# Optimization experiments

Measured on AMD Instinct MI355X. Metric: run time of the kernel, lower is better.

The kernel has to match this reference:

```python
import math
import jax, jax.numpy as jnp
import numpy as np

B, S, E, H, DK, L, NB, V, FF, C = 4, 2048, 512, 8, 64, 2, 4, 32000, 2048, 4


def _pos_encoding(seq_len, embed_dim):
    pos = np.arange(seq_len, dtype=np.float32)[:, None]
    div = np.exp(np.arange(0, embed_dim, 2, dtype=np.float32) * (-math.log(10000.0) / embed_dim))
    pe = np.zeros((seq_len, embed_dim), dtype=np.float32)
    pe[:, 0::2] = np.sin(pos * div)
    pe[:, 1::2] = np.cos(pos * div)
    return jnp.asarray(pe)


def _layernorm(x, g, b, eps=1e-5):
    m = jnp.mean(x, axis=-1, keepdims=True)
    v = jnp.mean((x - m) ** 2, axis=-1, keepdims=True)
    return (x - m) * jax.lax.rsqrt(v + eps) * g + b


def setup_inputs() -> dict:
    key = jax.random.key(0)
    ks = jax.random.split(key, 32)
    sd = 0.02
    inp = {
        "tokens": jax.random.randint(ks[0], (B, S), 0, V, dtype=jnp.int32),
        "emb": jax.random.normal(ks[1], (V, E), jnp.float32) * sd,
        # per-block stacked params (leading dim NB)
        "Wq": jax.random.normal(ks[2], (NB, E, E), jnp.float32) * sd,
        "Wk": jax.random.normal(ks[3], (NB, E, E), jnp.float32) * sd,
        "Wv": jax.random.normal(ks[4], (NB, E, E), jnp.float32) * sd,
        "Wo": jax.random.normal(ks[5], (NB, E, E), jnp.float32) * sd,
        # quantum per-head linear stacks: [NB, L, H, DK, DK] weights, [NB, L, H, DK] biases
        "qh_w": jax.random.normal(ks[6], (NB, L, H, DK, DK), jnp.float32) * 0.1,
        "qh_b": jax.random.normal(ks[7], (NB, L, H, DK), jnp.float32) * 0.01,
        "kh_w": jax.random.normal(ks[8], (NB, L, H, DK, DK), jnp.float32) * 0.1,
        "kh_b": jax.random.normal(ks[9], (NB, L, H, DK), jnp.float32) * 0.01,
        "vh_w": jax.random.normal(ks[10], (NB, L, H, DK, DK), jnp.float32) * 0.1,
        "vh_b": jax.random.normal(ks[11], (NB, L, H, DK), jnp.float32) * 0.01,
        "ln1_g": jnp.ones((NB, E), jnp.float32),
        "ln1_b": jnp.zeros((NB, E), jnp.float32),
        "ln2_g": jnp.ones((NB, E), jnp.float32),
        "ln2_b": jnp.zeros((NB, E), jnp.float32),
        "f_w1": jax.random.normal(ks[12], (NB, E, FF), jnp.float32) * sd,
        "f_b1": jnp.zeros((NB, FF), jnp.float32),
        "f_w2": jax.random.normal(ks[13], (NB, FF, E), jnp.float32) * sd,
        "f_b2": jnp.zeros((NB, E), jnp.float32),
        "cls_w": jax.random.normal(ks[14], (E, C), jnp.float32) * sd,
        "cls_b": jnp.zeros((C,), jnp.float32),
    }
    return inp


def _quantum_apply(h, w_stack, b_stack):
    # h: [B,H,S,DK]; w_stack: [L,H,DK,DK]; b_stack: [L,H,DK]
    for l in range(L):
        h = jnp.einsum("bhsd,hde->bhse", h, w_stack[l]) + b_stack[l][None, :, None, :]
    return h


def _block(x, Wq, Wk, Wv, Wo, qh_w, qh_b, kh_w, kh_b, vh_w, vh_b,
           ln1_g, ln1_b, ln2_g, ln2_b, f_w1, f_b1, f_w2, f_b2):
    b, s, _ = x.shape
    q = (x @ Wq).reshape(b, s, H, DK).transpose(0, 2, 1, 3)  # [B,H,S,DK]
    k = (x @ Wk).reshape(b, s, H, DK).transpose(0, 2, 1, 3)
    v = (x @ Wv).reshape(b, s, H, DK).transpose(0, 2, 1, 3)
    q = _quantum_apply(q, qh_w, qh_b)
    k = _quantum_apply(k, kh_w, kh_b)
    v = _quantum_apply(v, vh_w, vh_b)
    scores = jnp.einsum("bhqd,bhkd->bhqk", q, k) / math.sqrt(DK)
    attn = jax.nn.softmax(scores, axis=-1)
    out = jnp.einsum("bhqk,bhkd->bhqd", attn, v)
    out = out.transpose(0, 2, 1, 3).reshape(b, s, E) @ Wo
    x = _layernorm(x + out, ln1_g, ln1_b)
    ffn = jax.nn.relu(x @ f_w1 + f_b1) @ f_w2 + f_b2
    return _layernorm(x + ffn, ln2_g, ln2_b)


def reference(tokens, emb, Wq, Wk, Wv, Wo, qh_w, qh_b, kh_w, kh_b, vh_w, vh_b,
              ln1_g, ln1_b, ln2_g, ln2_b, f_w1, f_b1, f_w2, f_b2, cls_w, cls_b):
    x = emb[tokens]  # [B,S,E]
    x = x + _pos_encoding(S, E)[None]
    for i in range(NB):
        x = _block(x, Wq[i], Wk[i], Wv[i], Wo[i],
                   qh_w[i], qh_b[i], kh_w[i], kh_b[i], vh_w[i], vh_b[i],
                   ln1_g[i], ln1_b[i], ln2_g[i], ln2_b[i],
                   f_w1[i], f_b1[i], f_w2[i], f_b2[i])
    x = x.mean(axis=1)  # [B,E]
    return x @ cls_w + cls_b  # [B,C]
```

## Files before the change

### kernel.cpp

```cpp
#include <hip/hip_runtime.h>
#include <hip/hip_bf16.h>
#include <math.h>

#define BB 4
#define SS 2048
#define EE 512
#define HH 8
#define DKK 64
#define LL 2
#define NBB 4
#define FFF 2048
#define CC 4
#define NBSE ((size_t)BB * SS * EE)

typedef __attribute__((ext_vector_type(8))) short bf16x8;
typedef __attribute__((ext_vector_type(4))) float f32x4;
using bf16 = __hip_bfloat16;

__device__ __forceinline__ float fast_exp2(float x) { return __builtin_amdgcn_exp2f(x); }

__device__ __forceinline__ void gload16(const bf16* g, bf16* l) {
    __builtin_amdgcn_global_load_lds((const __attribute__((address_space(1))) void*)g,
                                     (__attribute__((address_space(3))) void*)l, 16, 0, 0);
}
__device__ __forceinline__ unsigned short bf16bits(float f) {
    bf16 h = __float2bfloat16(f);
    return *(unsigned short*)&h;
}

__global__ __launch_bounds__(256) void embed_kernel(const int* __restrict__ tokens,
                                                    const float* __restrict__ emb,
                                                    float* __restrict__ x,
                                                    bf16* __restrict__ xb) {
    int i = blockIdx.x * blockDim.x + threadIdx.x;
    int total = BB * SS * EE / 2;
    if (i >= total) return;
    int pi  = i & (EE / 2 - 1);
    int row = i >> 8;
    int s   = row & (SS - 1);
    int tok = tokens[row];
    int e0  = pi * 2;
    const float kln = 9.210340371976184f / (float)EE;
    float arg = (float)s * expf(-(float)e0 * kln);
    float2 ev = *(const float2*)(emb + (size_t)tok * EE + e0);
    float2 o;
    o.x = ev.x + sinf(arg);
    o.y = ev.y + cosf(arg);
    *(float2*)(x + (size_t)row * EE + e0) = o;
    xb[(size_t)row * EE + e0]     = __float2bfloat16(o.x);
    xb[(size_t)row * EE + e0 + 1] = __float2bfloat16(o.y);
}

__global__ __launch_bounds__(256) void transpose_to_bf16(const float* __restrict__ in,
                                                         bf16* __restrict__ out,
                                                         int K, int N,
                                                         size_t zstride, int row_off) {
    const float* src = in + (size_t)blockIdx.z * K * N;
    bf16* dst = out + (size_t)blockIdx.z * zstride;
    int r0 = blockIdx.y * 64, c0 = blockIdx.x * 64;
    __shared__ float tl[64][65];
    int t = threadIdx.x;
    int lr = t >> 4, lc = (t & 15) * 4;
#pragma unroll
    for (int i = 0; i < 4; i++) {
        float4 v = *(const float4*)(src + (size_t)(r0 + lr + i * 16) * N + c0 + lc);
        tl[lr + i * 16][lc + 0] = v.x;
        tl[lr + i * 16][lc + 1] = v.y;
        tl[lr + i * 16][lc + 2] = v.z;
        tl[lr + i * 16][lc + 3] = v.w;
    }
    __syncthreads();
#pragma unroll
    for (int i = 0; i < 4; i++) {
        int n = lr + i * 16;
#pragma unroll
        for (int j = 0; j < 4; j++)
            dst[(size_t)(row_off + c0 + n) * K + r0 + lc + j] = __float2bfloat16(tl[lc + j][n]);
    }
}

#define GF_RELU 1
#define GF_SCATTER3 2
#define GF_OUTBF16 4
__global__ __launch_bounds__(256) void gemm_bf16(const bf16* __restrict__ A,
                                                 const bf16* __restrict__ BT,
                                                 const float* __restrict__ bias,
                                                 void* __restrict__ C,
                                                 int M, int N, int K, int flags) {
    __shared__ __align__(16) bf16 Asm[128 * 32];
    __shared__ __align__(16) bf16 Bsm[128 * 32];
    int t = threadIdx.x;
    int l = t & 63, w = t >> 6;
    int nbx = gridDim.x;
    int lin = blockIdx.y * nbx + blockIdx.x;
    int cpx = (nbx * gridDim.y) >> 3;
    int swz = (lin & 7) * cpx + (lin >> 3);
    int bm = (swz / nbx) * 128, bn = (swz % nbx) * 128;
    int wr = (w >> 1) * 64, wc = (w & 1) * 64;
    int lr = l & 15, lg = l >> 4;
    int ca = w * 2;
    int sr = l >> 2, sk = (l & 3) * 8;
    const bf16* ga  = A  + (size_t)(bm + ca * 16 + sr) * K + sk;
    const bf16* ga2 = ga + (size_t)16 * K;
    const bf16* gb  = BT + (size_t)(bn + ca * 16 + sr) * K + sk;
    const bf16* gb2 = gb + (size_t)16 * K;

    f32x4 acc[4][4];
#pragma unroll
    for (int m = 0; m < 4; m++)
#pragma unroll
        for (int n = 0; n < 4; n++) acc[m][n] = (f32x4){0.f, 0.f, 0.f, 0.f};

    for (int k0 = 0; k0 < K; k0 += 32) {
        __syncthreads();
        gload16(ga + k0,  &Asm[ca * 512]);
        gload16(ga2 + k0, &Asm[ca * 512 + 512]);
        gload16(gb + k0,  &Bsm[ca * 512]);
        gload16(gb2 + k0, &Bsm[ca * 512 + 512]);
        __syncthreads();
        bf16x8 af[4], bfr[4];
#pragma unroll
        for (int m = 0; m < 4; m++)
            af[m] = *(const bf16x8*)&Asm[(wr + m * 16 + lr) * 32 + lg * 8];
#pragma unroll
        for (int n = 0; n < 4; n++)
            bfr[n] = *(const bf16x8*)&Bsm[(wc + n * 16 + lr) * 32 + lg * 8];
#pragma unroll
        for (int m = 0; m < 4; m++)
#pragma unroll
            for (int n = 0; n < 4; n++)
                acc[m][n] = __builtin_amdgcn_mfma_f32_16x16x32_bf16(af[m], bfr[n], acc[m][n], 0, 0, 0);
    }

#pragma unroll
    for (int m = 0; m < 4; m++) {
        int row = bm + wr + m * 16 + lg * 4;
#pragma unroll
        for (int n = 0; n < 4; n++) {
            int col = bn + wc + n * 16 + lr;
            float bv = bias ? bias[col] : 0.f;
#pragma unroll
            for (int r = 0; r < 4; r++) {
                float v = acc[m][n][r] + bv;
                if (flags & GF_RELU) v = fmaxf(v, 0.f);
                int rr = row + r;
                if (flags & GF_SCATTER3) {
                    int tsel = col >> 9;
                    int b = rr >> 11, s = rr & (SS - 1);
                    int h = (col >> 6) & 7, dk = col & 63;
                    ((bf16*)C)[tsel * NBSE + (((size_t)(b * HH + h) * SS + s) << 6) + dk] = __float2bfloat16(v);
                } else if (flags & GF_OUTBF16) {
                    ((bf16*)C)[(size_t)rr * N + col] = __float2bfloat16(v);
                } else {
                    ((float*)C)[(size_t)rr * N + col] = v;
                }
            }
        }
    }
}

__global__ __launch_bounds__(256) void gemm_bf16_m64(const bf16* __restrict__ A,
                                                     const bf16* __restrict__ BT,
                                                     const float* __restrict__ bias,
                                                     void* __restrict__ C,
                                                     int M, int N, int K, int flags) {
    __shared__ __align__(16) bf16 Asm[64 * 32];
    __shared__ __align__(16) bf16 Bsm[128 * 32];
    int t = threadIdx.x;
    int l = t & 63, w = t >> 6;
    int nbx = gridDim.x;
    int lin = blockIdx.y * nbx + blockIdx.x;
    int cpx = (nbx * gridDim.y) >> 3;
    int swz = (lin & 7) * cpx + (lin >> 3);
    int bm = (swz / nbx) * 64, bn = (swz % nbx) * 128;
    int wr = (w >> 1) * 32, wc = (w & 1) * 64;
    int lr = l & 15, lg = l >> 4;
    int ca = w * 2;
    int sr = l >> 2, sk = (l & 3) * 8;
    const bf16* ga  = A  + (size_t)(bm + w * 16 + sr) * K + sk;
    const bf16* gb  = BT + (size_t)(bn + ca * 16 + sr) * K + sk;
    const bf16* gb2 = gb + (size_t)16 * K;

    f32x4 acc[2][4];
#pragma unroll
    for (int m = 0; m < 2; m++)
#pragma unroll
        for (int n = 0; n < 4; n++) acc[m][n] = (f32x4){0.f, 0.f, 0.f, 0.f};

    for (int k0 = 0; k0 < K; k0 += 32) {
        __syncthreads();
        gload16(ga + k0,  &Asm[w * 512]);
        gload16(gb + k0,  &Bsm[ca * 512]);
        gload16(gb2 + k0, &Bsm[ca * 512 + 512]);
        __syncthreads();
        bf16x8 af[2], bfr[4];
#pragma unroll
        for (int m = 0; m < 2; m++)
            af[m] = *(const bf16x8*)&Asm[(wr + m * 16 + lr) * 32 + lg * 8];
#pragma unroll
        for (int n = 0; n < 4; n++)
            bfr[n] = *(const bf16x8*)&Bsm[(wc + n * 16 + lr) * 32 + lg * 8];
#pragma unroll
        for (int m = 0; m < 2; m++)
#pragma unroll
            for (int n = 0; n < 4; n++)
                acc[m][n] = __builtin_amdgcn_mfma_f32_16x16x32_bf16(af[m], bfr[n], acc[m][n], 0, 0, 0);
    }

#pragma unroll
    for (int m = 0; m < 2; m++) {
        int row = bm + wr + m * 16 + lg * 4;
#pragma unroll
        for (int n = 0; n < 4; n++) {
            int col = bn + wc + n * 16 + lr;
            float bv = bias ? bias[col] : 0.f;
#pragma unroll
            for (int r = 0; r < 4; r++) {
                float v = acc[m][n][r] + bv;
                if (flags & GF_RELU) v = fmaxf(v, 0.f);
                int rr = row + r;
                if (flags & GF_OUTBF16) {
                    ((bf16*)C)[(size_t)rr * N + col] = __float2bfloat16(v);
                } else {
                    ((float*)C)[(size_t)rr * N + col] = v;
                }
            }
        }
    }
}

__global__ __launch_bounds__(256) void quantum_mfma(bf16* __restrict__ qb, bf16* __restrict__ kb, bf16* __restrict__ vb,
                                                    bf16* __restrict__ vT,
                                                    const bf16* __restrict__ qwT, const bf16* __restrict__ kwT, const bf16* __restrict__ vwT,
                                                    const float* __restrict__ qbi, const float* __restrict__ kbi, const float* __restrict__ vbi) {
    __shared__ __align__(16) bf16 Hs[128 * 72];
    __shared__ __align__(16) bf16 W0s[64 * 72];
    __shared__ __align__(16) bf16 W1s[64 * 72];
    int z = blockIdx.z;
    bf16* hb       = z == 0 ? qb  : (z == 1 ? kb  : vb);
    const bf16* wT = z == 0 ? qwT : (z == 1 ? kwT : vwT);
    const float* bi = z == 0 ? qbi : (z == 1 ? kbi : vbi);
    int bh = blockIdx.y, h = bh & (HH - 1);
    int s0 = blockIdx.x * 128;
    int t = threadIdx.x, l = t & 63, w = t >> 6;
    int lr = l & 15, lg = l >> 4;
    bf16* base = hb + ((size_t)bh * SS + s0) * DKK;
    const bf16* w0p = wT + (size_t)h * 4096;
    const bf16* w1p = wT + (size_t)(HH + h) * 4096;
    {
        int r = t >> 1, dbase = (t & 1) * 32;
#pragma unroll
        for (int i = 0; i < 4; i++) {
            uint4 hv = *(const uint4*)(base + (size_t)r * 64 + dbase + i * 8);
            *(uint4*)&Hs[r * 72 + dbase + i * 8] = hv;
        }
        const bf16* wp = (t < 128) ? w0p : w1p;
        bf16* Ws = (t < 128) ? W0s : W1s;
        int tt = t & 127;
        int wr2 = tt >> 1, wd = (tt & 1) * 32;
#pragma unroll
        for (int i = 0; i < 4; i++) {
            uint4 wv = *(const uint4*)(wp + wr2 * 64 + wd + i * 8);
            *(uint4*)&Ws[wr2 * 72 + wd + i * 8] = wv;
        }
    }
    __syncthreads();
    f32x4 acc[2][4];
#pragma unroll
    for (int m = 0; m < 2; m++)
#pragma unroll
        for (int n = 0; n < 4; n++) acc[m][n] = (f32x4){0.f, 0.f, 0.f, 0.f};
    bf16x8 af[2][2];
#pragma unroll
    for (int m = 0; m < 2; m++)
#pragma unroll
        for (int ks = 0; ks < 2; ks++)
            af[m][ks] = *(const bf16x8*)&Hs[(w * 32 + m * 16 + lr) * 72 + ks * 32 + lg * 8];
#pragma unroll
    for (int n = 0; n < 4; n++)
#pragma unroll
        for (int ks = 0; ks < 2; ks++) {
            bf16x8 bfr = *(const bf16x8*)&W0s[(n * 16 + lr) * 72 + ks * 32 + lg * 8];
#pragma unroll
            for (int m = 0; m < 2; m++)
                acc[m][n] = __builtin_amdgcn_mfma_f32_16x16x32_bf16(af[m][ks], bfr, acc[m][n], 0, 0, 0);
        }
#pragma unroll
    for (int n = 0; n < 4; n++) {
        float b0 = bi[(size_t)h * 64 + n * 16 + lr];
#pragma unroll
        for (int m = 0; m < 2; m++)
#pragma unroll
            for (int r = 0; r < 4; r++)
                Hs[(w * 32 + m * 16 + lg * 4 + r) * 72 + n * 16 + lr] = __float2bfloat16(acc[m][n][r] + b0);
    }
    f32x4 acc2[2][4];
#pragma unroll
    for (int m = 0; m < 2; m++)
#pragma unroll
        for (int n = 0; n < 4; n++) acc2[m][n] = (f32x4){0.f, 0.f, 0.f, 0.f};
    bf16x8 af2[2][2];
#pragma unroll
    for (int m = 0; m < 2; m++)
#pragma unroll
        for (int ks = 0; ks < 2; ks++)
            af2[m][ks] = *(const bf16x8*)&Hs[(w * 32 + m * 16 + lr) * 72 + ks * 32 + lg * 8];
#pragma unroll
    for (int n = 0; n < 4; n++)
#pragma unroll
        for (int ks = 0; ks < 2; ks++) {
            bf16x8 bfr = *(const bf16x8*)&W1s[(n * 16 + lr) * 72 + ks * 32 + lg * 8];
#pragma unroll
            for (int m = 0; m < 2; m++)
                acc2[m][n] = __builtin_amdgcn_mfma_f32_16x16x32_bf16(af2[m][ks], bfr, acc2[m][n], 0, 0, 0);
        }
    if (z == 2) {
        __syncthreads();
        bf16* vt = Hs;
#pragma unroll
        for (int n = 0; n < 4; n++) {
            float b1 = bi[(size_t)(HH + h) * 64 + n * 16 + lr];
#pragma unroll
            for (int m = 0; m < 2; m++) {
                ushort4 pk;
                pk.x = bf16bits(acc2[m][n][0] + b1);
                pk.y = bf16bits(acc2[m][n][1] + b1);
                pk.z = bf16bits(acc2[m][n][2] + b1);
                pk.w = bf16bits(acc2[m][n][3] + b1);
                *(ushort4*)&vt[(n * 16 + lr) * 136 + w * 32 + m * 16 + lg * 4] = pk;
            }
        }
        __syncthreads();
        bf16* vbase = vT + (size_t)bh * DKK * SS + s0;
        int row = t >> 2, c0 = (t & 3) * 32;
#pragma unroll
        for (int i = 0; i < 4; i++)
            *(uint4*)(vbase + (size_t)row * SS + c0 + i * 8) = *(uint4*)&vt[row * 136 + c0 + i * 8];
    } else {
#pragma unroll
        for (int n = 0; n < 4; n++) {
            float b1 = bi[(size_t)(HH + h) * 64 + n * 16 + lr];
#pragma unroll
            for (int m = 0; m < 2; m++)
#pragma unroll
                for (int r = 0; r < 4; r++)
                    base[(size_t)(w * 32 + m * 16 + lg * 4 + r) * 64 + n * 16 + lr] = __float2bfloat16(acc2[m][n][r] + b1);
        }
    }
}

__global__ __launch_bounds__(512) __attribute__((amdgpu_waves_per_eu(6, 6)))
void attn_mfma(const bf16* __restrict__ q,
               const bf16* __restrict__ k,
               const bf16* __restrict__ vT,
               bf16* __restrict__ ao) {
    __shared__ __align__(16) bf16 Ksm[64 * 72];
    __shared__ __align__(16) bf16 Vtm[64 * 72];
    __shared__ __align__(16) bf16 Psm[8 * 16 * 68];
    int wg  = blockIdx.x;
    int nw  = (wg & 7) * 64 + (wg >> 3);
    int bh  = nw >> 4;
    int q0  = (nw & 15) * 128;
    int b = bh >> 3, hh = bh & 7;
    int t = threadIdx.x, l = t & 63, w = t >> 6;
    int lr = l & 15, lg = l >> 4;
    bf16* Pw = &Psm[w * 16 * 68];

    bf16x8 qf[2];
#pragma unroll
    for (int ks = 0; ks < 2; ks++)
        qf[ks] = *(const bf16x8*)(q + ((size_t)bh * SS + q0 + w * 16 + lr) * DKK + ks * 32 + lg * 8);

    float m_run[4] = {-INFINITY, -INFINITY, -INFINITY, -INFINITY};
    float l_run[4] = {0.f, 0.f, 0.f, 0.f};
    f32x4 accO[4];
#pragma unroll
    for (int j = 0; j < 4; j++) accO[j] = (f32x4){0.f, 0.f, 0.f, 0.f};

    const bf16* kbase = k  + (size_t)bh * SS * DKK;
    const bf16* vbase = vT + (size_t)bh * DKK * SS;
    int srow = t >> 3, scol = (t & 7) * 8;

    uint4 kreg, vreg;
    kreg = *(const uint4*)(kbase + (size_t)srow * DKK + scol);
    vreg = *(const uint4*)(vbase + (size_t)srow * SS + scol);

    const float SC = 0.180336879f;

    for (int kt = 0; kt < SS; kt += 64) {
        __syncthreads();
        *(uint4*)&Ksm[srow * 72 + scol] = kreg;
        *(uint4*)&Vtm[srow * 72 + scol] = vreg;
        __syncthreads();
        if (kt + 64 < SS) {
            kreg = *(const uint4*)(kbase + (size_t)(kt + 64 + srow) * DKK + scol);
            vreg = *(const uint4*)(vbase + (size_t)srow * SS + kt + 64 + scol);
        }

        f32x4 s[4];
#pragma unroll
        for (int n = 0; n < 4; n++) s[n] = (f32x4){0.f, 0.f, 0.f, 0.f};
        __builtin_amdgcn_s_setprio(1);
#pragma unroll
        for (int n = 0; n < 4; n++)
#pragma unroll
            for (int ks = 0; ks < 2; ks++) {
                bf16x8 kf = *(const bf16x8*)&Ksm[(n * 16 + lr) * 72 + ks * 32 + lg * 8];
                s[n] = __builtin_amdgcn_mfma_f32_16x16x32_bf16(qf[ks], kf, s[n], 0, 0, 0);
            }
        __builtin_amdgcn_s_setprio(0);

#pragma unroll
        for (int n = 0; n < 4; n++) s[n] *= SC;
        float tmax[4];
#pragma unroll
        for (int r = 0; r < 4; r++) {
            float mx = fmaxf(fmaxf(s[0][r], s[1][r]), fmaxf(s[2][r], s[3][r]));
            mx = fmaxf(mx, __shfl_xor(mx, 1, 16));
            mx = fmaxf(mx, __shfl_xor(mx, 2, 16));
            mx = fmaxf(mx, __shfl_xor(mx, 4, 16));
            mx = fmaxf(mx, __shfl_xor(mx, 8, 16));
            tmax[r] = mx;
        }
        bool ok = true;
#pragma unroll
        for (int r = 0; r < 4; r++) ok = ok && (tmax[r] <= m_run[r] + 8.f);
        if (!__all(ok)) {
#pragma unroll
            for (int r = 0; r < 4; r++) {
                float mn = fmaxf(m_run[r], tmax[r]);
                float fc = fast_exp2(m_run[r] - mn);
                m_run[r] = mn;
                l_run[r] *= fc;
#pragma unroll
                for (int j = 0; j < 4; j++) accO[j][r] *= fc;
            }
        }
        float lsum[4] = {0.f, 0.f, 0.f, 0.f};
#pragma unroll
        for (int n = 0; n < 4; n++)
#pragma unroll
            for (int r = 0; r < 4; r++) {
                float p = fast_exp2(s[n][r] - m_run[r]);
                lsum[r] += p;
                s[n][r] = p;
            }
#pragma unroll
        for (int r = 0; r < 4; r++) {
            float ls = lsum[r];
            ls += __shfl_xor(ls, 1, 16);
            ls += __shfl_xor(ls, 2, 16);
            ls += __shfl_xor(ls, 4, 16);
            ls += __shfl_xor(ls, 8, 16);
            l_run[r] += ls;
        }

#pragma unroll
        for (int n = 0; n < 4; n++)
#pragma unroll
            for (int r = 0; r < 4; r++)
                Pw[(lg * 4 + r) * 68 + n * 16 + lr] = __float2bfloat16(s[n][r]);

        bf16x8 pa[2];
#pragma unroll
        for (int ks = 0; ks < 2; ks++)
            pa[ks] = *(const bf16x8*)&Pw[lr * 68 + ks * 32 + lg * 8];
        __builtin_amdgcn_s_setprio(1);
#pragma unroll
        for (int j = 0; j < 4; j++)
#pragma unroll
            for (int ks = 0; ks < 2; ks++) {
                bf16x8 vb8 = *(const bf16x8*)&Vtm[(j * 16 + lr) * 72 + ks * 32 + lg * 8];
                accO[j] = __builtin_amdgcn_mfma_f32_16x16x32_bf16(pa[ks], vb8, accO[j], 0, 0, 0);
            }
        __builtin_amdgcn_s_setprio(0);
    }

    float inv[4];
#pragma unroll
    for (int r = 0; r < 4; r++) inv[r] = 1.f / l_run[r];
#pragma unroll
    for (int j = 0; j < 4; j++)
#pragma unroll
        for (int r = 0; r < 4; r++) {
            int row = q0 + w * 16 + lg * 4 + r;
            ao[((size_t)(b * SS) + row) * EE + hh * 64 + j * 16 + lr] = __float2bfloat16(accO[j][r] * inv[r]);
        }
}

__global__ __launch_bounds__(256) void ln_kernel(float* __restrict__ x,
                                                 const float* __restrict__ res,
                                                 const float* __restrict__ g,
                                                 const float* __restrict__ beta,
                                                 bf16* __restrict__ xb) {
    int row = blockIdx.x;
    int t = threadIdx.x;
    float* xr = x + (size_t)row * EE;
    const float* rr = res + (size_t)row * EE;
    float v0 = xr[t] + rr[t];
    float v1 = xr[t + 256] + rr[t + 256];
    __shared__ float red[4];
    float s = v0 + v1;
#pragma unroll
    for (int m = 1; m < 64; m <<= 1) s += __shfl_xor(s, m, 64);
    if ((t & 63) == 0) red[t >> 6] = s;
    __syncthreads();
    s = red[0] + red[1] + red[2] + red[3];
    float mean = s * (1.f / EE);
    float d0 = v0 - mean, d1 = v1 - mean;
    float qv = d0 * d0 + d1 * d1;
    __syncthreads();
#pragma unroll
    for (int m = 1; m < 64; m <<= 1) qv += __shfl_xor(qv, m, 64);
    if ((t & 63) == 0) red[t >> 6] = qv;
    __syncthreads();
    qv = red[0] + red[1] + red[2] + red[3];
    float rs = rsqrtf(qv * (1.f / EE) + 1e-5f);
    float o0 = d0 * rs * g[t] + beta[t];
    float o1 = d1 * rs * g[t + 256] + beta[t + 256];
    xr[t] = o0;
    xr[t + 256] = o1;
    xb[(size_t)row * EE + t] = __float2bfloat16(o0);
    xb[(size_t)row * EE + t + 256] = __float2bfloat16(o1);
}

__global__ __launch_bounds__(256) void meanpart_kernel(const float* __restrict__ x,
                                                       float* __restrict__ part) {
    int b = blockIdx.y, c = blockIdx.x;
    int t = threadIdx.x;
    float s0 = 0.f, s1 = 0.f;
    for (int s = c * 32; s < c * 32 + 32; s++) {
        const float* row = x + ((size_t)b * SS + s) * EE;
        s0 += row[t];
        s1 += row[t + 256];
    }
    part[(size_t)(b * 64 + c) * EE + t] = s0;
    part[(size_t)(b * 64 + c) * EE + t + 256] = s1;
}

__global__ __launch_bounds__(256) void meancls_kernel(const float* __restrict__ part,
                                                      const float* __restrict__ cw,
                                                      const float* __restrict__ cb,
                                                      float* __restrict__ out) {
    int b = blockIdx.x;
    int t = threadIdx.x;
    __shared__ float xm[EE];
    float s0 = 0.f, s1 = 0.f;
    for (int i = 0; i < 64; i++) {
        s0 += part[(size_t)(b * 64 + i) * EE + t];
        s1 += part[(size_t)(b * 64 + i) * EE + t + 256];
    }
    xm[t] = s0 * (1.f / SS);
    xm[t + 256] = s1 * (1.f / SS);
    __syncthreads();
    if (t < CC) {
        float acc = cb[t];
        for (int e = 0; e < EE; e++) acc += xm[e] * cw[e * CC + t];
        out[b * CC + t] = acc;
    }
}

extern "C" void kernel_launch(void* const* d_in, const int* in_sizes, int n_in,
                              void* d_out, int out_size, void* d_ws, size_t ws_size,
                              hipStream_t stream) {
    (void)in_sizes; (void)n_in; (void)out_size; (void)ws_size;
    const int*   tokens = (const int*)d_in[0];
    const float* emb    = (const float*)d_in[1];
    const float* Wq     = (const float*)d_in[2];
    const float* Wk     = (const float*)d_in[3];
    const float* Wv     = (const float*)d_in[4];
    const float* Wo     = (const float*)d_in[5];
    const float* qh_w   = (const float*)d_in[6];
    const float* qh_b   = (const float*)d_in[7];
    const float* kh_w   = (const float*)d_in[8];
    const float* kh_b   = (const float*)d_in[9];
    const float* vh_w   = (const float*)d_in[10];
    const float* vh_b   = (const float*)d_in[11];
    const float* ln1_g  = (const float*)d_in[12];
    const float* ln1_b  = (const float*)d_in[13];
    const float* ln2_g  = (const float*)d_in[14];
    const float* ln2_b  = (const float*)d_in[15];
    const float* f_w1   = (const float*)d_in[16];
    const float* f_b1   = (const float*)d_in[17];
    const float* f_w2   = (const float*)d_in[18];
    const float* f_b2   = (const float*)d_in[19];
    const float* cls_w  = (const float*)d_in[20];
    const float* cls_b  = (const float*)d_in[21];

    const size_t nBSF = (size_t)BB * SS * FFF;
    float* x    = (float*)d_ws;
    float* t0   = x + NBSE;
    float* part = t0 + NBSE;
    bf16* xb    = (bf16*)(part + (size_t)BB * 64 * EE);
    bf16* qb    = xb + NBSE;
    bf16* kb    = qb + NBSE;
    bf16* vb    = kb + NBSE;
    bf16* vTb   = vb + NBSE;
    bf16* ao    = vTb + NBSE;
    bf16* ffnb  = ao + NBSE;
    bf16* WqkvT = ffnb + nBSF;
    bf16* WoT   = WqkvT + (size_t)NBB * 3 * EE * EE;
    bf16* fw1T  = WoT + (size_t)NBB * EE * EE;
    bf16* fw2T  = fw1T + (size_t)NBB * EE * FFF;
    bf16* qhT   = fw2T + (size_t)NBB * EE * FFF;
    bf16* khT   = qhT + (size_t)NBB * LL * HH * DKK * DKK;
    bf16* vhT   = khT + (size_t)NBB * LL * HH * DKK * DKK;

    const int M = BB * SS;
    const size_t zQKV = (size_t)3 * EE * EE;

    transpose_to_bf16<<<dim3(EE / 64, EE / 64, NBB), 256, 0, stream>>>(Wq, WqkvT, EE, EE, zQKV, 0);
    transpose_to_bf16<<<dim3(EE / 64, EE / 64, NBB), 256, 0, stream>>>(Wk, WqkvT, EE, EE, zQKV, EE);
    transpose_to_bf16<<<dim3(EE / 64, EE / 64, NBB), 256, 0, stream>>>(Wv, WqkvT, EE, EE, zQKV, 2 * EE);
    transpose_to_bf16<<<dim3(EE / 64, EE / 64, NBB), 256, 0, stream>>>(Wo, WoT, EE, EE, (size_t)EE * EE, 0);
    transpose_to_bf16<<<dim3(FFF / 64, EE / 64, NBB), 256, 0, stream>>>(f_w1, fw1T, EE, FFF, (size_t)EE * FFF, 0);
    transpose_to_bf16<<<dim3(EE / 64, FFF / 64, NBB), 256, 0, stream>>>(f_w2, fw2T, FFF, EE, (size_t)EE * FFF, 0);
    transpose_to_bf16<<<dim3(1, 1, NBB * LL * HH), 256, 0, stream>>>(qh_w, qhT, DKK, DKK, (size_t)DKK * DKK, 0);
    transpose_to_bf16<<<dim3(1, 1, NBB * LL * HH), 256, 0, stream>>>(kh_w, khT, DKK, DKK, (size_t)DKK * DKK, 0);
    transpose_to_bf16<<<dim3(1, 1, NBB * LL * HH), 256, 0, stream>>>(vh_w, vhT, DKK, DKK, (size_t)DKK * DKK, 0);

    embed_kernel<<<(BB * SS * EE / 2 + 255) / 256, 256, 0, stream>>>(tokens, emb, x, xb);

    for (int blk = 0; blk < NBB; blk++) {
        dim3 gEE64(EE / 128, M / 64);
        dim3 gQKV(3 * EE / 128, M / 128);
        dim3 gFF(FFF / 128, M / 128);
        const size_t wE = (size_t)blk * EE * EE;
        const size_t qwOff = (size_t)blk * LL * HH * DKK * DKK;
        const size_t qbOff = (size_t)blk * LL * HH * DKK;

        gemm_bf16<<<gQKV, 256, 0, stream>>>(xb, WqkvT + blk * zQKV, nullptr, qb, M, 3 * EE, EE, GF_SCATTER3);

        quantum_mfma<<<dim3(SS / 128, BB * HH, 3), 256, 0, stream>>>(
            qb, kb, vb, vTb, qhT + qwOff, khT + qwOff, vhT + qwOff,
            qh_b + qbOff, kh_b + qbOff, vh_b + qbOff);

        attn_mfma<<<dim3(512), 512, 0, stream>>>(qb, kb, vTb, ao);

        gemm_bf16_m64<<<gEE64, 256, 0, stream>>>(ao, WoT + wE, nullptr, t0, M, EE, EE, 0);
        ln_kernel<<<M, 256, 0, stream>>>(x, t0, ln1_g + blk * EE, ln1_b + blk * EE, xb);

        gemm_bf16<<<gFF, 256, 0, stream>>>(xb, fw1T + (size_t)blk * EE * FFF, f_b1 + blk * FFF, ffnb, M, FFF, EE, GF_RELU | GF_OUTBF16);
        gemm_bf16_m64<<<gEE64, 256, 0, stream>>>(ffnb, fw2T + (size_t)blk * EE * FFF, f_b2 + blk * EE, t0, M, EE, FFF, 0);
        ln_kernel<<<M, 256, 0, stream>>>(x, t0, ln2_g + blk * EE, ln2_b + blk * EE, xb);
    }

    meanpart_kernel<<<dim3(64, BB), 256, 0, stream>>>(x, part);
    meancls_kernel<<<BB, 256, 0, stream>>>(part, cls_w, cls_b, (float*)d_out);
}
```

Measured before the change: 1.173 ms.

## Split attention over two key halves and merge partials in a combine kernel

The attention kernel now splits the key sequence into two halves along a second grid dimension. Each block writes a normalized partial output in bf16 plus its running max and sum, and a new combine kernel merges the two partials with softmax rescaling before writing the head-interleaved output. This doubles the number of workgroups so more of the GPU can be occupied, and the occupancy hint is raised to 8 waves per EU. The cost is an extra kernel launch, extra global traffic for the partials, and an extra bf16 rounding of the partial outputs.

```diff
diff --git a/kernel.cpp b/kernel.cpp
--- a/kernel.cpp
+++ b/kernel.cpp
@@ -12,6 +12,7 @@
 #define FFF 2048
 #define CC 4
 #define NBSE ((size_t)BB * SS * EE)
+#define NQ ((size_t)BB * HH * SS)
 
 typedef __attribute__((ext_vector_type(8))) short bf16x8;
 typedef __attribute__((ext_vector_type(4))) float f32x4;
@@ -26,6 +27,10 @@
 __device__ __forceinline__ unsigned short bf16bits(float f) {
     bf16 h = __float2bfloat16(f);
     return *(unsigned short*)&h;
+}
+__device__ __forceinline__ float bits2f(unsigned short u) {
+    unsigned int x = ((unsigned int)u) << 16;
+    return *(float*)&x;
 }
 
 __global__ __launch_bounds__(256) void embed_kernel(const int* __restrict__ tokens,
@@ -349,19 +354,21 @@
     }
 }
 
-__global__ __launch_bounds__(512) __attribute__((amdgpu_waves_per_eu(6, 6)))
+__global__ __launch_bounds__(512) __attribute__((amdgpu_waves_per_eu(8, 8)))
 void attn_mfma(const bf16* __restrict__ q,
                const bf16* __restrict__ k,
                const bf16* __restrict__ vT,
-               bf16* __restrict__ ao) {
+               bf16* __restrict__ opart,
+               float2* __restrict__ ml) {
     __shared__ __align__(16) bf16 Ksm[64 * 72];
     __shared__ __align__(16) bf16 Vtm[64 * 72];
     __shared__ __align__(16) bf16 Psm[8 * 16 * 68];
     int wg  = blockIdx.x;
+    int kz  = blockIdx.y;
+    int k0  = kz << 10;
     int nw  = (wg & 7) * 64 + (wg >> 3);
     int bh  = nw >> 4;
     int q0  = (nw & 15) * 128;
-    int b = bh >> 3, hh = bh & 7;
     int t = threadIdx.x, l = t & 63, w = t >> 6;
     int lr = l & 15, lg = l >> 4;
     bf16* Pw = &Psm[w * 16 * 68];
@@ -382,17 +389,17 @@
     int srow = t >> 3, scol = (t & 7) * 8;
 
     uint4 kreg, vreg;
-    kreg = *(const uint4*)(kbase + (size_t)srow * DKK + scol);
-    vreg = *(const uint4*)(vbase + (size_t)srow * SS + scol);
+    kreg = *(const uint4*)(kbase + (size_t)(k0 + srow) * DKK + scol);
+    vreg = *(const uint4*)(vbase + (size_t)srow * SS + k0 + scol);
 
     const float SC = 0.180336879f;
 
-    for (int kt = 0; kt < SS; kt += 64) {
+    for (int kt = k0; kt < k0 + 1024; kt += 64) {
         __syncthreads();
         *(uint4*)&Ksm[srow * 72 + scol] = kreg;
         *(uint4*)&Vtm[srow * 72 + scol] = vreg;
         __syncthreads();
-        if (kt + 64 < SS) {
+        if (kt + 64 < k0 + 1024) {
             kreg = *(const uint4*)(kbase + (size_t)(kt + 64 + srow) * DKK + scol);
             vreg = *(const uint4*)(vbase + (size_t)srow * SS + kt + 64 + scol);
         }
@@ -479,13 +486,42 @@
     float inv[4];
 #pragma unroll
     for (int r = 0; r < 4; r++) inv[r] = 1.f / l_run[r];
+    bf16* obase = opart + ((size_t)kz * NQ + (size_t)bh * SS + q0) * DKK;
 #pragma unroll
     for (int j = 0; j < 4; j++)
 #pragma unroll
-        for (int r = 0; r < 4; r++) {
-            int row = q0 + w * 16 + lg * 4 + r;
-            ao[((size_t)(b * SS) + row) * EE + hh * 64 + j * 16 + lr] = __float2bfloat16(accO[j][r] * inv[r]);
-        }
+        for (int r = 0; r < 4; r++)
+            obase[(size_t)(w * 16 + lg * 4 + r) * DKK + j * 16 + lr] = __float2bfloat16(accO[j][r] * inv[r]);
+    if (lr == 0) {
+#pragma unroll
+        for (int r = 0; r < 4; r++)
+            ml[(size_t)kz * NQ + (size_t)bh * SS + q0 + w * 16 + lg * 4 + r] = make_float2(m_run[r], l_run[r]);
+    }
+}
+
+__global__ __launch_bounds__(256) void attn_combine(const bf16* __restrict__ opart,
+                                                    const float2* __restrict__ ml,
+                                                    bf16* __restrict__ ao) {
+    int gidx = blockIdx.x * 256 + threadIdx.x;
+    int row = gidx >> 4;
+    int d0  = (gidx & 15) * 4;
+    float2 ml0 = ml[row];
+    float2 ml1 = ml[NQ + row];
+    float m = fmaxf(ml0.x, ml1.x);
+    float w0 = fast_exp2(ml0.x - m) * ml0.y;
+    float w1 = fast_exp2(ml1.x - m) * ml1.y;
+    float inv = 1.f / (w0 + w1);
+    w0 *= inv; w1 *= inv;
+    ushort4 a = *(const ushort4*)(opart + (size_t)row * DKK + d0);
+    ushort4 bb = *(const ushort4*)(opart + NQ * DKK + (size_t)row * DKK + d0);
+    ushort4 o;
+    o.x = bf16bits(w0 * bits2f(a.x) + w1 * bits2f(bb.x));
+    o.y = bf16bits(w0 * bits2f(a.y) + w1 * bits2f(bb.y));
+    o.z = bf16bits(w0 * bits2f(a.z) + w1 * bits2f(bb.z));
+    o.w = bf16bits(w0 * bits2f(a.w) + w1 * bits2f(bb.w));
+    int bh = row >> 11, s = row & (SS - 1);
+    int b = bh >> 3, hh = bh & 7;
+    *(ushort4*)(ao + ((size_t)(b * SS + s)) * EE + hh * 64 + d0) = o;
 }
 
 __global__ __launch_bounds__(256) void ln_kernel(float* __restrict__ x,
@@ -605,6 +641,8 @@
     bf16* qhT   = fw2T + (size_t)NBB * EE * FFF;
     bf16* khT   = qhT + (size_t)NBB * LL * HH * DKK * DKK;
     bf16* vhT   = khT + (size_t)NBB * LL * HH * DKK * DKK;
+    bf16* opart = vhT + (size_t)NBB * LL * HH * DKK * DKK;
+    float2* mlb = (float2*)(opart + (size_t)2 * NQ * DKK);
 
     const int M = BB * SS;
     const size_t zQKV = (size_t)3 * EE * EE;
@@ -635,7 +673,8 @@
             qb, kb, vb, vTb, qhT + qwOff, khT + qwOff, vhT + qwOff,
             qh_b + qbOff, kh_b + qbOff, vh_b + qbOff);
 
-        attn_mfma<<<dim3(512), 512, 0, stream>>>(qb, kb, vTb, ao);
+        attn_mfma<<<dim3(512, 2), 512, 0, stream>>>(qb, kb, vTb, opart, mlb);
+        attn_combine<<<(int)(NQ * 16 / 256), 256, 0, stream>>>(opart, mlb, ao);
 
         gemm_bf16_m64<<<gEE64, 256, 0, stream>>>(ao, WoT + wE, nullptr, t0, M, EE, EE, 0);
         ln_kernel<<<M, 256, 0, stream>>>(x, t0, ln1_g + blk * EE, ln1_b + blk * EE, xb);
```

Result: slower. 1.467 ms (+25.1%).
